# Optimization experiments

Hardware: AMD Instinct MI355X
Metric: run time of the kernel (lower is better)

Reference implementation:

```python
import jax, jax.numpy as jnp
import numpy as np

MAX_DIST = 8
GUIDANCE_WEIGHT = 0.4
EPS_MAG = 1e-6
EPS_COS = 1e-8
EPS_WSUM = 1e-8


def setup_inputs() -> dict:
    key = jax.random.key(0)
    k1, k2 = jax.random.split(key)
    embeddings = jax.random.normal(k1, (4, 2048, 1024), dtype=jnp.float32)
    guidance_trajectories = jax.random.normal(k2, (512, 1024), dtype=jnp.float32)
    return {"embeddings": embeddings, "guidance_trajectories": guidance_trajectories}


def reference(embeddings, guidance_trajectories):
    B, S, D = embeddings.shape
    W = min(MAX_DIST, S - 1)  # fixed max window size

    # consecutive-token trajectory vectors: diffs[t] = emb[t+1] - emb[t]
    diffs = embeddings[:, 1:, :] - embeddings[:, :-1, :]          # [B, S-1, D]

    # sliding windows of the last W diffs ending at pos-1
    pos = jnp.arange(S)[:, None]                                  # [S, 1]
    k = jnp.arange(W)[None, :]                                    # [1, W]
    idx = pos - W + k                                             # diff index per slot
    valid = (idx >= 0) & (pos >= 1)                               # [S, W]
    windows = diffs[:, jnp.clip(idx, 0, S - 2), :]                # [B, S, W, D]

    # torch.linspace(0.1, 1.0, w) weights, per-position window size w = min(pos, W);
    # valid entries occupy the last w slots of the W-wide window.
    w = jnp.minimum(pos, W)                                       # [S, 1]
    j = k - (W - w)                                               # local index within window
    lin = jnp.where(w > 1, 0.1 + 0.9 * j / jnp.maximum(w - 1, 1), 0.1)
    pos_weights = jnp.where(valid, lin, 0.0).astype(embeddings.dtype)  # [S, W]

    # normalize trajectory vectors, zero where magnitude <= 1e-6
    mag = jnp.linalg.norm(windows, axis=-1, keepdims=True)        # [B, S, W, 1]
    is_valid_mag = mag > EPS_MAG
    normed = jnp.where(is_valid_mag, windows / jnp.where(is_valid_mag, mag, 1.0), 0.0)

    mag_weights = jnp.tanh(mag * 2.0)                             # [B, S, W, 1]
    combined = pos_weights[None, :, :, None] * mag_weights        # [B, S, W, 1]

    # guidance influence: softmax over cosine similarity to guidance bank
    g_norm = jnp.linalg.norm(guidance_trajectories, axis=-1)      # [G]
    a_norm = jnp.linalg.norm(normed, axis=-1)                     # [B, S, W]
    dots = jnp.einsum('bswd,gd->bswg', normed, guidance_trajectories)
    sims = dots / (jnp.maximum(a_norm, EPS_COS)[..., None] * jnp.maximum(g_norm, EPS_COS))
    g_weights = jax.nn.softmax(sims * 2.0, axis=-1)               # [B, S, W, G]
    influence = jnp.einsum('bswg,gd->bswd', g_weights, guidance_trajectories)
    blended = (1.0 - GUIDANCE_WEIGHT) * normed + GUIDANCE_WEIGHT * influence

    weight_sum = jnp.maximum(combined.sum(axis=2), EPS_WSUM)      # [B, S, 1]
    trajectories = (blended * combined).sum(axis=2) / weight_sum  # [B, S, D]
    return trajectories
```

## Files before the change

kernel.cpp:

```cpp
#include <hip/hip_runtime.h>
#include <math.h>

#define B_ 4
#define S_ 2048
#define D_ 1024
#define G_ 512
#define T_ 2047
#define R_ 8188
#define RPAD 8192
#define MT 32
#define ABST 520

typedef __attribute__((ext_vector_type(8))) short short8;
typedef __attribute__((ext_vector_type(4))) short s16x4;
typedef __attribute__((ext_vector_type(4))) float f32x4;
typedef __attribute__((ext_vector_type(4))) unsigned short u16x4;

#define WSOFF_RG2  0u
#define WSOFF_MAGW 2048u
#define WSOFF_RMAG 34816u
#define WSOFF_BP1  67584u
#define WSOFF_BP2  1116160u
#define WSOFF_NH   2164736u
#define WSOFF_IH   18941952u

__device__ inline short to_bf16(float f) {
    union { float f; unsigned u; } v; v.f = f;
    unsigned r = v.u + 0x7fffu + ((v.u >> 16) & 1u);
    return (short)(r >> 16);
}
__device__ inline float fb(unsigned short h) {
    union { unsigned u; float f; } v;
    v.u = ((unsigned)h) << 16;
    return v.f;
}

__global__ __launch_bounds__(256) void prep_kernel(const float* __restrict__ guid,
                                                   float* __restrict__ rg2,
                                                   short8* __restrict__ Bp1,
                                                   short8* __restrict__ Bp2) {
    int bid = blockIdx.x, tid = threadIdx.x;
    if (bid < 128) {
        int wave = tid >> 6, lane = tid & 63;
        int g = bid * 4 + wave;
        const float4* gp = (const float4*)(guid + (size_t)g * D_);
        float ss = 0.f;
#pragma unroll
        for (int i = 0; i < 4; ++i) {
            float4 v = gp[lane + 64 * i];
            ss += v.x * v.x + v.y * v.y + v.z * v.z + v.w * v.w;
        }
#pragma unroll
        for (int m = 32; m >= 1; m >>= 1) ss += __shfl_xor(ss, m, 64);
        if (lane == 0) rg2[g] = 2.0f / fmaxf(sqrtf(ss), 1e-8f);
#pragma unroll
        for (int h = 0; h < 2; ++h) {
            int kg = lane + 64 * h;
            const float* src = guid + (size_t)g * D_ + kg * 8;
            short8 v;
#pragma unroll
            for (int j = 0; j < 8; ++j) v[j] = to_bf16(src[j]);
            Bp1[(size_t)kg * G_ + g] = v;
        }
    } else {
        int gg = bid - 128;
#pragma unroll
        for (int dd = 0; dd < 4; ++dd) {
            int d = tid + 256 * dd;
            short8 v;
#pragma unroll
            for (int j = 0; j < 8; ++j) v[j] = to_bf16(guid[(size_t)(gg * 8 + j) * D_ + d]);
            Bp2[(size_t)gg * D_ + d] = v;
        }
    }
}

__global__ __launch_bounds__(1024, 4) void fused_kernel(const float* __restrict__ emb,
                                                        const short8* __restrict__ Bp1,
                                                        const short8* __restrict__ Bp2,
                                                        const float* __restrict__ rg2,
                                                        float* __restrict__ magw,
                                                        float* __restrict__ rmagA,
                                                        short* __restrict__ normh,
                                                        short* __restrict__ inflh) {
    __shared__ short AB[MT][ABST];
    __shared__ float rg2s[G_];
    __shared__ float pred[MT][16];
    __shared__ float redmx[MT], redrs[MT];
    __shared__ float rmagS[MT];

    const int tid = threadIdx.x;
    const int wave = tid >> 6, lane = tid & 63;
    const int l15 = lane & 15, quad = lane >> 4;
    const int r0 = blockIdx.x * MT;

    if (tid < G_) rg2s[tid] = rg2[tid];

    float4 hx0[2][2], hx1[2][2];
    float ssp[2];
    int Rrow[2];
#pragma unroll
    for (int i = 0; i < 2; ++i) {
        int rr = wave * 2 + i;
        int R = r0 + rr;
        Rrow[i] = R;
        if (R < R_) {
            int b = R / T_;
            int t = R - b * T_;
            const float4* p = (const float4*)(emb + ((size_t)b * S_ + t) * D_);
            float ss = 0.f;
            short* nb = normh + (size_t)R * D_ + 4 * lane;
#pragma unroll
            for (int j = 0; j < 2; ++j) {
                float4 x0 = p[lane + 64 * j];
                float4 x1 = p[lane + 64 * j + 256];
                float4 dv = make_float4(x1.x - x0.x, x1.y - x0.y, x1.z - x0.z, x1.w - x0.w);
                ss += dv.x * dv.x + dv.y * dv.y + dv.z * dv.z + dv.w * dv.w;
                s16x4 h;
                h[0] = to_bf16(dv.x); h[1] = to_bf16(dv.y);
                h[2] = to_bf16(dv.z); h[3] = to_bf16(dv.w);
                *(s16x4*)(nb + 256 * j) = h;
                *(s16x4*)&AB[rr][4 * lane + 256 * j] = h;
            }
            ssp[i] = ss;
#pragma unroll
            for (int j = 0; j < 2; ++j) {
                hx0[i][j] = p[lane + 64 * (j + 2)];
                hx1[i][j] = p[lane + 64 * (j + 2) + 256];
            }
        } else {
            s16x4 z = (s16x4)0;
            *(s16x4*)&AB[rr][4 * lane] = z;
            *(s16x4*)&AB[rr][4 * lane + 256] = z;
            ssp[i] = 0.f;
#pragma unroll
            for (int j = 0; j < 2; ++j) {
                hx0[i][j] = make_float4(0.f, 0.f, 0.f, 0.f);
                hx1[i][j] = make_float4(0.f, 0.f, 0.f, 0.f);
            }
        }
    }
    __builtin_amdgcn_sched_barrier(0);
    asm volatile("s_waitcnt lgkmcnt(0)" ::: "memory");
    __builtin_amdgcn_s_barrier();

    f32x4 acc1[2][2];
#pragma unroll
    for (int mt = 0; mt < 2; ++mt)
#pragma unroll
        for (int nt = 0; nt < 2; ++nt) acc1[mt][nt] = (f32x4)0.f;
    {
        const short8* Bb = Bp1 + (size_t)quad * G_ + wave * 32 + l15;
        short8 bc0 = Bb[0], bc1 = Bb[16], bn0, bn1;
        for (int ks = 0; ks < 16; ++ks) {
            if (ks < 15) {
                const short8* Bx = Bb + (size_t)(ks + 1) * 4 * G_;
                bn0 = Bx[0]; bn1 = Bx[16];
            }
            short8 a0 = *(const short8*)&AB[l15][ks * 32 + quad * 8];
            short8 a1 = *(const short8*)&AB[16 + l15][ks * 32 + quad * 8];
            acc1[0][0] = __builtin_amdgcn_mfma_f32_16x16x32_bf16(a0, bc0, acc1[0][0], 0, 0, 0);
            acc1[0][1] = __builtin_amdgcn_mfma_f32_16x16x32_bf16(a0, bc1, acc1[0][1], 0, 0, 0);
            acc1[1][0] = __builtin_amdgcn_mfma_f32_16x16x32_bf16(a1, bc0, acc1[1][0], 0, 0, 0);
            acc1[1][1] = __builtin_amdgcn_mfma_f32_16x16x32_bf16(a1, bc1, acc1[1][1], 0, 0, 0);
            bc0 = bn0; bc1 = bn1;
        }
    }

    s16x4 holdh[2][2];
#pragma unroll
    for (int i = 0; i < 2; ++i) {
        int R = Rrow[i];
        int rr = wave * 2 + i;
        float ss = ssp[i];
        if (R < R_) {
            short* nb = normh + (size_t)R * D_ + 4 * lane;
#pragma unroll
            for (int j = 0; j < 2; ++j) {
                float4 dv = make_float4(hx1[i][j].x - hx0[i][j].x, hx1[i][j].y - hx0[i][j].y,
                                        hx1[i][j].z - hx0[i][j].z, hx1[i][j].w - hx0[i][j].w);
                ss += dv.x * dv.x + dv.y * dv.y + dv.z * dv.z + dv.w * dv.w;
                s16x4 h;
                h[0] = to_bf16(dv.x); h[1] = to_bf16(dv.y);
                h[2] = to_bf16(dv.z); h[3] = to_bf16(dv.w);
                *(s16x4*)(nb + 256 * (j + 2)) = h;
                holdh[i][j] = h;
            }
        } else {
            holdh[i][0] = (s16x4)0; holdh[i][1] = (s16x4)0;
        }
#pragma unroll
        for (int m = 32; m >= 1; m >>= 1) ss += __shfl_xor(ss, m, 64);
        float mag = sqrtf(ss);
        float rmag = (mag > 1e-6f) ? (1.0f / mag) : 0.0f;
        if (lane == 0) {
            rmagS[rr] = rmag;
            if (R < R_) { magw[R] = tanhf(2.0f * mag); rmagA[R] = rmag; }
        }
    }
    __syncthreads();
#pragma unroll
    for (int i = 0; i < 2; ++i) {
        int rr = wave * 2 + i;
        *(s16x4*)&AB[rr][4 * lane] = holdh[i][0];
        *(s16x4*)&AB[rr][4 * lane + 256] = holdh[i][1];
    }
    __syncthreads();

    {
        const short8* Bb = Bp1 + (size_t)(64 + quad) * G_ + wave * 32 + l15;
        short8 bc0 = Bb[0], bc1 = Bb[16], bn0, bn1;
        for (int ks = 0; ks < 16; ++ks) {
            if (ks < 15) {
                const short8* Bx = Bb + (size_t)(ks + 1) * 4 * G_;
                bn0 = Bx[0]; bn1 = Bx[16];
            }
            short8 a0 = *(const short8*)&AB[l15][ks * 32 + quad * 8];
            short8 a1 = *(const short8*)&AB[16 + l15][ks * 32 + quad * 8];
            acc1[0][0] = __builtin_amdgcn_mfma_f32_16x16x32_bf16(a0, bc0, acc1[0][0], 0, 0, 0);
            acc1[0][1] = __builtin_amdgcn_mfma_f32_16x16x32_bf16(a0, bc1, acc1[0][1], 0, 0, 0);
            acc1[1][0] = __builtin_amdgcn_mfma_f32_16x16x32_bf16(a1, bc0, acc1[1][0], 0, 0, 0);
            acc1[1][1] = __builtin_amdgcn_mfma_f32_16x16x32_bf16(a1, bc1, acc1[1][1], 0, 0, 0);
            bc0 = bn0; bc1 = bn1;
        }
    }

    {
        float rmv[2][4];
#pragma unroll
        for (int mt = 0; mt < 2; ++mt)
#pragma unroll
            for (int r2 = 0; r2 < 4; ++r2) rmv[mt][r2] = rmagS[mt * 16 + quad * 4 + r2];
        float pmax[2][4];
#pragma unroll
        for (int mt = 0; mt < 2; ++mt)
#pragma unroll
            for (int r2 = 0; r2 < 4; ++r2) pmax[mt][r2] = -1e30f;
#pragma unroll
        for (int mt = 0; mt < 2; ++mt)
#pragma unroll
            for (int nt = 0; nt < 2; ++nt) {
                float rgv = rg2s[wave * 32 + nt * 16 + l15];
#pragma unroll
                for (int r2 = 0; r2 < 4; ++r2) {
                    float lg = acc1[mt][nt][r2] * rgv * rmv[mt][r2];
                    acc1[mt][nt][r2] = lg;
                    pmax[mt][r2] = fmaxf(pmax[mt][r2], lg);
                }
            }
#pragma unroll
        for (int m = 8; m >= 1; m >>= 1)
#pragma unroll
            for (int mt = 0; mt < 2; ++mt)
#pragma unroll
                for (int r2 = 0; r2 < 4; ++r2)
                    pmax[mt][r2] = fmaxf(pmax[mt][r2], __shfl_xor(pmax[mt][r2], m, 16));
        if (l15 == 0) {
#pragma unroll
            for (int mt = 0; mt < 2; ++mt)
#pragma unroll
                for (int r2 = 0; r2 < 4; ++r2)
                    pred[mt * 16 + quad * 4 + r2][wave] = pmax[mt][r2];
        }
        __syncthreads();
        if (tid < MT) {
            float m = pred[tid][0];
#pragma unroll
            for (int w2 = 1; w2 < 16; ++w2) m = fmaxf(m, pred[tid][w2]);
            redmx[tid] = m;
        }
        __syncthreads();
        float psum[2][4];
#pragma unroll
        for (int mt = 0; mt < 2; ++mt)
#pragma unroll
            for (int r2 = 0; r2 < 4; ++r2) psum[mt][r2] = 0.f;
#pragma unroll
        for (int mt = 0; mt < 2; ++mt)
#pragma unroll
            for (int nt = 0; nt < 2; ++nt)
#pragma unroll
                for (int r2 = 0; r2 < 4; ++r2) {
                    float e = __expf(acc1[mt][nt][r2] - redmx[mt * 16 + quad * 4 + r2]);
                    acc1[mt][nt][r2] = e;
                    psum[mt][r2] += e;
                }
#pragma unroll
        for (int m = 8; m >= 1; m >>= 1)
#pragma unroll
            for (int mt = 0; mt < 2; ++mt)
#pragma unroll
                for (int r2 = 0; r2 < 4; ++r2)
                    psum[mt][r2] += __shfl_xor(psum[mt][r2], m, 16);
        if (l15 == 0) {
#pragma unroll
            for (int mt = 0; mt < 2; ++mt)
#pragma unroll
                for (int r2 = 0; r2 < 4; ++r2)
                    pred[mt * 16 + quad * 4 + r2][wave] = psum[mt][r2];
        }
        __syncthreads();
        if (tid < MT) {
            float s = 0.f;
#pragma unroll
            for (int w2 = 0; w2 < 16; ++w2) s += pred[tid][w2];
            redrs[tid] = 1.0f / s;
        }
        __syncthreads();
#pragma unroll
        for (int mt = 0; mt < 2; ++mt)
#pragma unroll
            for (int nt = 0; nt < 2; ++nt)
#pragma unroll
                for (int r2 = 0; r2 < 4; ++r2) {
                    int row = mt * 16 + quad * 4 + r2;
                    AB[row][wave * 32 + nt * 16 + l15] =
                        to_bf16(acc1[mt][nt][r2] * redrs[row]);
                }
    }
    __syncthreads();

    f32x4 acc2[2][4];
#pragma unroll
    for (int mt = 0; mt < 2; ++mt)
#pragma unroll
        for (int nt = 0; nt < 4; ++nt) acc2[mt][nt] = (f32x4)0.f;
    {
        const short8* Bb = Bp2 + (size_t)quad * D_ + wave * 64 + l15;
        short8 bc[4], bn[4];
#pragma unroll
        for (int nt = 0; nt < 4; ++nt) bc[nt] = Bb[nt * 16];
        for (int ks = 0; ks < 16; ++ks) {
            if (ks < 15) {
                const short8* Bx = Bb + (size_t)(ks + 1) * 4 * D_;
#pragma unroll
                for (int nt = 0; nt < 4; ++nt) bn[nt] = Bx[nt * 16];
            }
            short8 a0 = *(const short8*)&AB[l15][ks * 32 + quad * 8];
            short8 a1 = *(const short8*)&AB[16 + l15][ks * 32 + quad * 8];
#pragma unroll
            for (int nt = 0; nt < 4; ++nt) {
                acc2[0][nt] = __builtin_amdgcn_mfma_f32_16x16x32_bf16(a0, bc[nt], acc2[0][nt], 0, 0, 0);
                acc2[1][nt] = __builtin_amdgcn_mfma_f32_16x16x32_bf16(a1, bc[nt], acc2[1][nt], 0, 0, 0);
            }
#pragma unroll
            for (int nt = 0; nt < 4; ++nt) bc[nt] = bn[nt];
        }
    }

#pragma unroll
    for (int mt = 0; mt < 2; ++mt)
#pragma unroll
        for (int nt = 0; nt < 4; ++nt) {
            int d = wave * 64 + nt * 16 + l15;
#pragma unroll
            for (int r2 = 0; r2 < 4; ++r2) {
                int R = r0 + mt * 16 + quad * 4 + r2;
                if (R < R_) inflh[(size_t)R * D_ + d] = to_bf16(acc2[mt][nt][r2]);
            }
        }
}

__global__ __launch_bounds__(256) void combine_kernel(const float* __restrict__ magw,
                                                      const float* __restrict__ rmagA,
                                                      const unsigned short* __restrict__ normh,
                                                      const unsigned short* __restrict__ inflh,
                                                      float* __restrict__ out) {
    int blk = blockIdx.x;
    int b = blk >> 7;
    int s0 = (blk & 127) * 16;
    int d0 = threadIdx.x * 4;
    size_t rbase = (size_t)b * T_;

    f32x4 ring[8]; float mring[8];
#pragma unroll
    for (int j = 0; j < 8; ++j) { ring[j] = (f32x4)0.f; mring[j] = 0.f; }

#define BLEND(n4_, i4_, ns_, dst_)                                       \
    {                                                                    \
        dst_[0] = ns_ * fb(n4_[0]) + 0.4f * fb(i4_[0]);                  \
        dst_[1] = ns_ * fb(n4_[1]) + 0.4f * fb(i4_[1]);                  \
        dst_[2] = ns_ * fb(n4_[2]) + 0.4f * fb(i4_[2]);                  \
        dst_[3] = ns_ * fb(n4_[3]) + 0.4f * fb(i4_[3]);                  \
    }

    if (s0 != 0) {
#pragma unroll
        for (int j = 0; j < 8; ++j) {
            int t = s0 - 8 + j;
            size_t off = (rbase + t) * D_ + d0;
            u16x4 n4 = *(const u16x4*)(normh + off);
            u16x4 i4 = *(const u16x4*)(inflh + off);
            float ns = 0.6f * rmagA[rbase + t];
            BLEND(n4, i4, ns, ring[j]);
            mring[j] = magw[rbase + t];
        }
#pragma unroll
        for (int i = 0; i < 16; ++i) {
            u16x4 pn = (u16x4)0, pi = (u16x4)0; float pm = 0.f, pr = 0.f;
            if (i < 15) {
                int t = s0 + i;
                size_t off = (rbase + t) * D_ + d0;
                pn = *(const u16x4*)(normh + off);
                pi = *(const u16x4*)(inflh + off);
                pm = magw[rbase + t];
                pr = rmagA[rbase + t];
            }
            f32x4 acc = (f32x4)0.f; float wsum = 0.f;
#pragma unroll
            for (int a = 1; a <= 8; ++a) {
                int slot = (i - a) & 7;
                const float lin = 0.1f + (0.9f / 7.0f) * (float)(8 - a);
                float wt = lin * mring[slot];
                acc[0] += wt * ring[slot][0]; acc[1] += wt * ring[slot][1];
                acc[2] += wt * ring[slot][2]; acc[3] += wt * ring[slot][3];
                wsum += wt;
            }
            float rws = 1.0f / fmaxf(wsum, 1e-8f);
            f32x4 o; o[0] = acc[0] * rws; o[1] = acc[1] * rws; o[2] = acc[2] * rws; o[3] = acc[3] * rws;
            *(f32x4*)&out[((size_t)b * S_ + s0 + i) * D_ + d0] = o;
            if (i < 15) {
                float ns = 0.6f * pr;
                BLEND(pn, pi, ns, ring[i & 7]);
                mring[i & 7] = pm;
            }
        }
    } else {
#pragma unroll
        for (int i = 0; i < 16; ++i) {
            u16x4 pn = (u16x4)0, pi = (u16x4)0; float pm = 0.f, pr = 0.f;
            if (i < 15) {
                int t = i;
                size_t off = (rbase + t) * D_ + d0;
                pn = *(const u16x4*)(normh + off);
                pi = *(const u16x4*)(inflh + off);
                pm = magw[rbase + t];
                pr = rmagA[rbase + t];
            }
            const int w = (i < 8) ? i : 8;
            f32x4 acc = (f32x4)0.f; float wsum = 0.f;
            if (w > 0) {
                const float rw = (w > 1) ? 0.9f / (float)(w - 1) : 0.0f;
#pragma unroll
                for (int a = 1; a <= 8; ++a) {
                    if (a <= w) {
                        int slot = (i - a) & 7;
                        float lin = 0.1f + rw * (float)(w - a);
                        float wt = lin * mring[slot];
                        acc[0] += wt * ring[slot][0]; acc[1] += wt * ring[slot][1];
                        acc[2] += wt * ring[slot][2]; acc[3] += wt * ring[slot][3];
                        wsum += wt;
                    }
                }
            }
            float rws = 1.0f / fmaxf(wsum, 1e-8f);
            f32x4 o; o[0] = acc[0] * rws; o[1] = acc[1] * rws; o[2] = acc[2] * rws; o[3] = acc[3] * rws;
            *(f32x4*)&out[((size_t)b * S_ + i) * D_ + d0] = o;
            if (i < 15) {
                float ns = 0.6f * pr;
                BLEND(pn, pi, ns, ring[i & 7]);
                mring[i & 7] = pm;
            }
        }
    }
#undef BLEND
}

extern "C" void kernel_launch(void* const* d_in, const int* in_sizes, int n_in,
                              void* d_out, int out_size, void* d_ws, size_t ws_size,
                              hipStream_t stream) {
    const float* emb  = (const float*)d_in[0];
    const float* guid = (const float*)d_in[1];
    float* out = (float*)d_out;
    char* ws = (char*)d_ws;

    float*  rg2   = (float*)(ws + WSOFF_RG2);
    float*  magw  = (float*)(ws + WSOFF_MAGW);
    float*  rmagA = (float*)(ws + WSOFF_RMAG);
    short8* Bp1   = (short8*)(ws + WSOFF_BP1);
    short8* Bp2   = (short8*)(ws + WSOFF_BP2);
    short*  normh = (short*)(ws + WSOFF_NH);
    short*  inflh = (short*)(ws + WSOFF_IH);

    prep_kernel<<<192, 256, 0, stream>>>(guid, rg2, Bp1, Bp2);
    fused_kernel<<<RPAD / MT, 1024, 0, stream>>>(emb, Bp1, Bp2, rg2, magw, rmagA, normh, inflh);
    combine_kernel<<<B_ * 128, 256, 0, stream>>>(magw, rmagA, (const unsigned short*)normh,
                                                 (const unsigned short*)inflh, out);
}
```

Baseline: 127.0 us.

## Drop softmax max pass, deepen GEMM prefetch, defer normalization, halve combine tile

The softmax no longer subtracts a row max, because the logits are cosine similarities times two and so stay bounded. This removes one cross-wave reduction and two block barriers. The row-sum reciprocal is now applied to the second GEMM's output rather than to the probabilities. Both GEMMs get deeper register prefetch of the B operand (four stages for the first, two for the second), and the remaining half of the embedding loads is issued after the first GEMM's prefetch. The combine kernel uses 8-row tiles with twice as many blocks and a software-pipelined load/blend sequence, at the cost of more halo reloads.

```diff
diff --git a/kernel.cpp b/kernel.cpp
--- a/kernel.cpp
+++ b/kernel.cpp
@@ -34,6 +34,16 @@
     v.u = ((unsigned)h) << 16;
     return v.f;
 }
+__device__ inline f32x4 MF(short8 a, short8 b, f32x4 c) {
+    return __builtin_amdgcn_mfma_f32_16x16x32_bf16(a, b, c, 0, 0, 0);
+}
+
+#define RAWBAR() do {                                            \
+    __builtin_amdgcn_sched_barrier(0);                           \
+    asm volatile("s_waitcnt lgkmcnt(0)" ::: "memory");           \
+    __builtin_amdgcn_s_barrier();                                \
+    __builtin_amdgcn_sched_barrier(0);                           \
+} while (0)
 
 __global__ __launch_bounds__(256) void prep_kernel(const float* __restrict__ guid,
                                                    float* __restrict__ rg2,
@@ -74,6 +84,12 @@
         }
     }
 }
+
+#define G1Q(ksv, q)  {                                                        \
+    short8 a0 = *(const short8*)&AB[l15][(ksv) * 32 + quad * 8];              \
+    short8 a1 = *(const short8*)&AB[16 + l15][(ksv) * 32 + quad * 8];         \
+    acc1[0][0] = MF(a0, q[0], acc1[0][0]); acc1[0][1] = MF(a0, q[1], acc1[0][1]); \
+    acc1[1][0] = MF(a1, q[0], acc1[1][0]); acc1[1][1] = MF(a1, q[1], acc1[1][1]); }
 
 __global__ __launch_bounds__(1024, 4) void fused_kernel(const float* __restrict__ emb,
                                                         const short8* __restrict__ Bp1,
@@ -86,7 +102,7 @@
     __shared__ short AB[MT][ABST];
     __shared__ float rg2s[G_];
     __shared__ float pred[MT][16];
-    __shared__ float redmx[MT], redrs[MT];
+    __shared__ float redrs[MT];
     __shared__ float rmagS[MT];
 
     const int tid = threadIdx.x;
@@ -96,7 +112,7 @@
 
     if (tid < G_) rg2s[tid] = rg2[tid];
 
-    float4 hx0[2][2], hx1[2][2];
+    const float4* prow[2];
     float ssp[2];
     int Rrow[2];
 #pragma unroll
@@ -104,11 +120,12 @@
         int rr = wave * 2 + i;
         int R = r0 + rr;
         Rrow[i] = R;
+        float ss = 0.f;
         if (R < R_) {
             int b = R / T_;
             int t = R - b * T_;
             const float4* p = (const float4*)(emb + ((size_t)b * S_ + t) * D_);
-            float ss = 0.f;
+            prow[i] = p;
             short* nb = normh + (size_t)R * D_ + 4 * lane;
 #pragma unroll
             for (int j = 0; j < 2; ++j) {
@@ -122,48 +139,51 @@
                 *(s16x4*)(nb + 256 * j) = h;
                 *(s16x4*)&AB[rr][4 * lane + 256 * j] = h;
             }
-            ssp[i] = ss;
-#pragma unroll
-            for (int j = 0; j < 2; ++j) {
-                hx0[i][j] = p[lane + 64 * (j + 2)];
-                hx1[i][j] = p[lane + 64 * (j + 2) + 256];
-            }
         } else {
+            prow[i] = (const float4*)emb;
             s16x4 z = (s16x4)0;
             *(s16x4*)&AB[rr][4 * lane] = z;
             *(s16x4*)&AB[rr][4 * lane + 256] = z;
-            ssp[i] = 0.f;
-#pragma unroll
-            for (int j = 0; j < 2; ++j) {
-                hx0[i][j] = make_float4(0.f, 0.f, 0.f, 0.f);
-                hx1[i][j] = make_float4(0.f, 0.f, 0.f, 0.f);
-            }
-        }
-    }
-    __builtin_amdgcn_sched_barrier(0);
-    asm volatile("s_waitcnt lgkmcnt(0)" ::: "memory");
-    __builtin_amdgcn_s_barrier();
+        }
+        ssp[i] = ss;
+    }
+    RAWBAR();
 
     f32x4 acc1[2][2];
 #pragma unroll
     for (int mt = 0; mt < 2; ++mt)
 #pragma unroll
         for (int nt = 0; nt < 2; ++nt) acc1[mt][nt] = (f32x4)0.f;
+
+    float4 hx0[2][2], hx1[2][2];
     {
         const short8* Bb = Bp1 + (size_t)quad * G_ + wave * 32 + l15;
-        short8 bc0 = Bb[0], bc1 = Bb[16], bn0, bn1;
-        for (int ks = 0; ks < 16; ++ks) {
-            if (ks < 15) {
-                const short8* Bx = Bb + (size_t)(ks + 1) * 4 * G_;
-                bn0 = Bx[0]; bn1 = Bx[16];
-            }
-            short8 a0 = *(const short8*)&AB[l15][ks * 32 + quad * 8];
-            short8 a1 = *(const short8*)&AB[16 + l15][ks * 32 + quad * 8];
-            acc1[0][0] = __builtin_amdgcn_mfma_f32_16x16x32_bf16(a0, bc0, acc1[0][0], 0, 0, 0);
-            acc1[0][1] = __builtin_amdgcn_mfma_f32_16x16x32_bf16(a0, bc1, acc1[0][1], 0, 0, 0);
-            acc1[1][0] = __builtin_amdgcn_mfma_f32_16x16x32_bf16(a1, bc0, acc1[1][0], 0, 0, 0);
-            acc1[1][1] = __builtin_amdgcn_mfma_f32_16x16x32_bf16(a1, bc1, acc1[1][1], 0, 0, 0);
-            bc0 = bn0; bc1 = bn1;
+        short8 q0[2], q1[2], q2[2], q3[2];
+        q0[0] = Bb[0];          q0[1] = Bb[16];
+        q1[0] = Bb[4 * G_];     q1[1] = Bb[4 * G_ + 16];
+        q2[0] = Bb[8 * G_];     q2[1] = Bb[8 * G_ + 16];
+        q3[0] = Bb[12 * G_];    q3[1] = Bb[12 * G_ + 16];
+#pragma unroll
+        for (int i = 0; i < 2; ++i) {
+            if (Rrow[i] < R_) {
+#pragma unroll
+                for (int j = 0; j < 2; ++j) {
+                    hx0[i][j] = prow[i][lane + 64 * (j + 2)];
+                    hx1[i][j] = prow[i][lane + 64 * (j + 2) + 256];
+                }
+            } else {
+                hx0[i][0] = make_float4(0.f, 0.f, 0.f, 0.f);
+                hx0[i][1] = make_float4(0.f, 0.f, 0.f, 0.f);
+                hx1[i][0] = make_float4(0.f, 0.f, 0.f, 0.f);
+                hx1[i][1] = make_float4(0.f, 0.f, 0.f, 0.f);
+            }
+        }
+#pragma unroll
+        for (int k4 = 0; k4 < 16; k4 += 4) {
+            G1Q(k4 + 0, q0); if (k4 < 12) { q0[0] = Bb[(k4 + 4) * 4 * G_]; q0[1] = Bb[(k4 + 4) * 4 * G_ + 16]; }
+            G1Q(k4 + 1, q1); if (k4 < 12) { q1[0] = Bb[(k4 + 5) * 4 * G_]; q1[1] = Bb[(k4 + 5) * 4 * G_ + 16]; }
+            G1Q(k4 + 2, q2); if (k4 < 12) { q2[0] = Bb[(k4 + 6) * 4 * G_]; q2[1] = Bb[(k4 + 6) * 4 * G_ + 16]; }
+            G1Q(k4 + 3, q3); if (k4 < 12) { q3[0] = Bb[(k4 + 7) * 4 * G_]; q3[1] = Bb[(k4 + 7) * 4 * G_ + 16]; }
         }
     }
 
@@ -198,32 +218,35 @@
             if (R < R_) { magw[R] = tanhf(2.0f * mag); rmagA[R] = rmag; }
         }
     }
-    __syncthreads();
+    RAWBAR();
 #pragma unroll
     for (int i = 0; i < 2; ++i) {
         int rr = wave * 2 + i;
         *(s16x4*)&AB[rr][4 * lane] = holdh[i][0];
         *(s16x4*)&AB[rr][4 * lane + 256] = holdh[i][1];
     }
-    __syncthreads();
+    RAWBAR();
 
     {
         const short8* Bb = Bp1 + (size_t)(64 + quad) * G_ + wave * 32 + l15;
-        short8 bc0 = Bb[0], bc1 = Bb[16], bn0, bn1;
-        for (int ks = 0; ks < 16; ++ks) {
-            if (ks < 15) {
-                const short8* Bx = Bb + (size_t)(ks + 1) * 4 * G_;
-                bn0 = Bx[0]; bn1 = Bx[16];
-            }
-            short8 a0 = *(const short8*)&AB[l15][ks * 32 + quad * 8];
-            short8 a1 = *(const short8*)&AB[16 + l15][ks * 32 + quad * 8];
-            acc1[0][0] = __builtin_amdgcn_mfma_f32_16x16x32_bf16(a0, bc0, acc1[0][0], 0, 0, 0);
-            acc1[0][1] = __builtin_amdgcn_mfma_f32_16x16x32_bf16(a0, bc1, acc1[0][1], 0, 0, 0);
-            acc1[1][0] = __builtin_amdgcn_mfma_f32_16x16x32_bf16(a1, bc0, acc1[1][0], 0, 0, 0);
-            acc1[1][1] = __builtin_amdgcn_mfma_f32_16x16x32_bf16(a1, bc1, acc1[1][1], 0, 0, 0);
-            bc0 = bn0; bc1 = bn1;
-        }
-    }
+        short8 q0[2], q1[2], q2[2], q3[2];
+        q0[0] = Bb[0];          q0[1] = Bb[16];
+        q1[0] = Bb[4 * G_];     q1[1] = Bb[4 * G_ + 16];
+        q2[0] = Bb[8 * G_];     q2[1] = Bb[8 * G_ + 16];
+        q3[0] = Bb[12 * G_];    q3[1] = Bb[12 * G_ + 16];
+#pragma unroll
+        for (int k4 = 0; k4 < 16; k4 += 4) {
+            G1Q(k4 + 0, q0); if (k4 < 12) { q0[0] = Bb[(k4 + 4) * 4 * G_]; q0[1] = Bb[(k4 + 4) * 4 * G_ + 16]; }
+            G1Q(k4 + 1, q1); if (k4 < 12) { q1[0] = Bb[(k4 + 5) * 4 * G_]; q1[1] = Bb[(k4 + 5) * 4 * G_ + 16]; }
+            G1Q(k4 + 2, q2); if (k4 < 12) { q2[0] = Bb[(k4 + 6) * 4 * G_]; q2[1] = Bb[(k4 + 6) * 4 * G_ + 16]; }
+            G1Q(k4 + 3, q3); if (k4 < 12) { q3[0] = Bb[(k4 + 7) * 4 * G_]; q3[1] = Bb[(k4 + 7) * 4 * G_ + 16]; }
+        }
+    }
+
+    const short8* Bb2 = Bp2 + (size_t)quad * D_ + wave * 64 + l15;
+    short8 c0[4];
+#pragma unroll
+    for (int nt = 0; nt < 4; ++nt) c0[nt] = Bb2[nt * 16];
 
     {
         float rmv[2][4];
@@ -231,11 +254,11 @@
         for (int mt = 0; mt < 2; ++mt)
 #pragma unroll
             for (int r2 = 0; r2 < 4; ++r2) rmv[mt][r2] = rmagS[mt * 16 + quad * 4 + r2];
-        float pmax[2][4];
+        float psum[2][4];
 #pragma unroll
         for (int mt = 0; mt < 2; ++mt)
 #pragma unroll
-            for (int r2 = 0; r2 < 4; ++r2) pmax[mt][r2] = -1e30f;
+            for (int r2 = 0; r2 < 4; ++r2) psum[mt][r2] = 0.f;
 #pragma unroll
         for (int mt = 0; mt < 2; ++mt)
 #pragma unroll
@@ -243,48 +266,11 @@
                 float rgv = rg2s[wave * 32 + nt * 16 + l15];
 #pragma unroll
                 for (int r2 = 0; r2 < 4; ++r2) {
-                    float lg = acc1[mt][nt][r2] * rgv * rmv[mt][r2];
-                    acc1[mt][nt][r2] = lg;
-                    pmax[mt][r2] = fmaxf(pmax[mt][r2], lg);
-                }
-            }
-#pragma unroll
-        for (int m = 8; m >= 1; m >>= 1)
-#pragma unroll
-            for (int mt = 0; mt < 2; ++mt)
-#pragma unroll
-                for (int r2 = 0; r2 < 4; ++r2)
-                    pmax[mt][r2] = fmaxf(pmax[mt][r2], __shfl_xor(pmax[mt][r2], m, 16));
-        if (l15 == 0) {
-#pragma unroll
-            for (int mt = 0; mt < 2; ++mt)
-#pragma unroll
-                for (int r2 = 0; r2 < 4; ++r2)
-                    pred[mt * 16 + quad * 4 + r2][wave] = pmax[mt][r2];
-        }
-        __syncthreads();
-        if (tid < MT) {
-            float m = pred[tid][0];
-#pragma unroll
-            for (int w2 = 1; w2 < 16; ++w2) m = fmaxf(m, pred[tid][w2]);
-            redmx[tid] = m;
-        }
-        __syncthreads();
-        float psum[2][4];
-#pragma unroll
-        for (int mt = 0; mt < 2; ++mt)
-#pragma unroll
-            for (int r2 = 0; r2 < 4; ++r2) psum[mt][r2] = 0.f;
-#pragma unroll
-        for (int mt = 0; mt < 2; ++mt)
-#pragma unroll
-            for (int nt = 0; nt < 2; ++nt)
-#pragma unroll
-                for (int r2 = 0; r2 < 4; ++r2) {
-                    float e = __expf(acc1[mt][nt][r2] - redmx[mt * 16 + quad * 4 + r2]);
+                    float e = __expf(acc1[mt][nt][r2] * rgv * rmv[mt][r2]);
                     acc1[mt][nt][r2] = e;
                     psum[mt][r2] += e;
                 }
+            }
 #pragma unroll
         for (int m = 8; m >= 1; m >>= 1)
 #pragma unroll
@@ -292,6 +278,15 @@
 #pragma unroll
                 for (int r2 = 0; r2 < 4; ++r2)
                     psum[mt][r2] += __shfl_xor(psum[mt][r2], m, 16);
+        RAWBAR();
+#pragma unroll
+        for (int mt = 0; mt < 2; ++mt)
+#pragma unroll
+            for (int nt = 0; nt < 2; ++nt)
+#pragma unroll
+                for (int r2 = 0; r2 < 4; ++r2)
+                    AB[mt * 16 + quad * 4 + r2][wave * 32 + nt * 16 + l15] =
+                        to_bf16(acc1[mt][nt][r2]);
         if (l15 == 0) {
 #pragma unroll
             for (int mt = 0; mt < 2; ++mt)
@@ -299,26 +294,14 @@
                 for (int r2 = 0; r2 < 4; ++r2)
                     pred[mt * 16 + quad * 4 + r2][wave] = psum[mt][r2];
         }
-        __syncthreads();
-        if (tid < MT) {
-            float s = 0.f;
-#pragma unroll
-            for (int w2 = 0; w2 < 16; ++w2) s += pred[tid][w2];
-            redrs[tid] = 1.0f / s;
-        }
-        __syncthreads();
-#pragma unroll
-        for (int mt = 0; mt < 2; ++mt)
-#pragma unroll
-            for (int nt = 0; nt < 2; ++nt)
-#pragma unroll
-                for (int r2 = 0; r2 < 4; ++r2) {
-                    int row = mt * 16 + quad * 4 + r2;
-                    AB[row][wave * 32 + nt * 16 + l15] =
-                        to_bf16(acc1[mt][nt][r2] * redrs[row]);
-                }
-    }
-    __syncthreads();
+    }
+    RAWBAR();
+    if (tid < MT) {
+        float s = 0.f;
+#pragma unroll
+        for (int w2 = 0; w2 < 16; ++w2) s += pred[tid][w2];
+        redrs[tid] = 1.0f / s;
+    }
 
     f32x4 acc2[2][4];
 #pragma unroll
@@ -326,27 +309,40 @@
 #pragma unroll
         for (int nt = 0; nt < 4; ++nt) acc2[mt][nt] = (f32x4)0.f;
     {
-        const short8* Bb = Bp2 + (size_t)quad * D_ + wave * 64 + l15;
-        short8 bc[4], bn[4];
-#pragma unroll
-        for (int nt = 0; nt < 4; ++nt) bc[nt] = Bb[nt * 16];
-        for (int ks = 0; ks < 16; ++ks) {
-            if (ks < 15) {
-                const short8* Bx = Bb + (size_t)(ks + 1) * 4 * D_;
-#pragma unroll
-                for (int nt = 0; nt < 4; ++nt) bn[nt] = Bx[nt * 16];
-            }
-            short8 a0 = *(const short8*)&AB[l15][ks * 32 + quad * 8];
-            short8 a1 = *(const short8*)&AB[16 + l15][ks * 32 + quad * 8];
-#pragma unroll
-            for (int nt = 0; nt < 4; ++nt) {
-                acc2[0][nt] = __builtin_amdgcn_mfma_f32_16x16x32_bf16(a0, bc[nt], acc2[0][nt], 0, 0, 0);
-                acc2[1][nt] = __builtin_amdgcn_mfma_f32_16x16x32_bf16(a1, bc[nt], acc2[1][nt], 0, 0, 0);
-            }
-#pragma unroll
-            for (int nt = 0; nt < 4; ++nt) bc[nt] = bn[nt];
-        }
-    }
+        short8 c1[4];
+#pragma unroll
+        for (int nt = 0; nt < 4; ++nt) c1[nt] = Bb2[4 * D_ + nt * 16];
+#pragma unroll
+        for (int k2 = 0; k2 < 16; k2 += 2) {
+            {
+                short8 a0 = *(const short8*)&AB[l15][k2 * 32 + quad * 8];
+                short8 a1 = *(const short8*)&AB[16 + l15][k2 * 32 + quad * 8];
+#pragma unroll
+                for (int nt = 0; nt < 4; ++nt) {
+                    acc2[0][nt] = MF(a0, c0[nt], acc2[0][nt]);
+                    acc2[1][nt] = MF(a1, c0[nt], acc2[1][nt]);
+                }
+                if (k2 < 14) {
+#pragma unroll
+                    for (int nt = 0; nt < 4; ++nt) c0[nt] = Bb2[(k2 + 2) * 4 * D_ + nt * 16];
+                }
+            }
+            {
+                short8 a0 = *(const short8*)&AB[l15][(k2 + 1) * 32 + quad * 8];
+                short8 a1 = *(const short8*)&AB[16 + l15][(k2 + 1) * 32 + quad * 8];
+#pragma unroll
+                for (int nt = 0; nt < 4; ++nt) {
+                    acc2[0][nt] = MF(a0, c1[nt], acc2[0][nt]);
+                    acc2[1][nt] = MF(a1, c1[nt], acc2[1][nt]);
+                }
+                if (k2 < 14) {
+#pragma unroll
+                    for (int nt = 0; nt < 4; ++nt) c1[nt] = Bb2[(k2 + 3) * 4 * D_ + nt * 16];
+                }
+            }
+        }
+    }
+    RAWBAR();
 
 #pragma unroll
     for (int mt = 0; mt < 2; ++mt)
@@ -355,8 +351,9 @@
             int d = wave * 64 + nt * 16 + l15;
 #pragma unroll
             for (int r2 = 0; r2 < 4; ++r2) {
-                int R = r0 + mt * 16 + quad * 4 + r2;
-                if (R < R_) inflh[(size_t)R * D_ + d] = to_bf16(acc2[mt][nt][r2]);
+                int row = mt * 16 + quad * 4 + r2;
+                int R = r0 + row;
+                if (R < R_) inflh[(size_t)R * D_ + d] = to_bf16(acc2[mt][nt][r2] * redrs[row]);
             }
         }
 }
@@ -367,77 +364,75 @@
                                                       const unsigned short* __restrict__ inflh,
                                                       float* __restrict__ out) {
     int blk = blockIdx.x;
-    int b = blk >> 7;
-    int s0 = (blk & 127) * 16;
+    int b = blk >> 8;
+    int s0 = (blk & 255) * 8;
     int d0 = threadIdx.x * 4;
     size_t rbase = (size_t)b * T_;
+    float* ob = out + ((size_t)b * S_ + s0) * D_ + d0;
 
     f32x4 ring[8]; float mring[8];
 #pragma unroll
     for (int j = 0; j < 8; ++j) { ring[j] = (f32x4)0.f; mring[j] = 0.f; }
 
-#define BLEND(n4_, i4_, ns_, dst_)                                       \
-    {                                                                    \
-        dst_[0] = ns_ * fb(n4_[0]) + 0.4f * fb(i4_[0]);                  \
-        dst_[1] = ns_ * fb(n4_[1]) + 0.4f * fb(i4_[1]);                  \
-        dst_[2] = ns_ * fb(n4_[2]) + 0.4f * fb(i4_[2]);                  \
-        dst_[3] = ns_ * fb(n4_[3]) + 0.4f * fb(i4_[3]);                  \
-    }
+#define CLOAD(t_, N_, I_, M_, RV_) {                                     \
+        size_t off_ = (rbase + (t_)) * D_ + d0;                          \
+        N_ = *(const u16x4*)(normh + off_);                              \
+        I_ = *(const u16x4*)(inflh + off_);                              \
+        M_ = magw[rbase + (t_)];                                         \
+        RV_ = rmagA[rbase + (t_)]; }
+
+#define CBLEND(slot_, N_, I_, M_, RV_) {                                 \
+        float ns_ = 0.6f * (RV_);                                        \
+        ring[slot_][0] = ns_ * fb(N_[0]) + 0.4f * fb(I_[0]);             \
+        ring[slot_][1] = ns_ * fb(N_[1]) + 0.4f * fb(I_[1]);             \
+        ring[slot_][2] = ns_ * fb(N_[2]) + 0.4f * fb(I_[2]);             \
+        ring[slot_][3] = ns_ * fb(N_[3]) + 0.4f * fb(I_[3]);             \
+        mring[slot_] = (M_); }
+
+#define CTAPS(i_) {                                                      \
+        f32x4 acc = (f32x4)0.f; float wsum = 0.f;                        \
+        _Pragma("unroll")                                                \
+        for (int a = 1; a <= 8; ++a) {                                   \
+            int slot = ((i_) - a) & 7;                                   \
+            float lin = 0.1f + (0.9f / 7.0f) * (float)(8 - a);           \
+            float wt = lin * mring[slot];                                \
+            acc[0] += wt * ring[slot][0]; acc[1] += wt * ring[slot][1];  \
+            acc[2] += wt * ring[slot][2]; acc[3] += wt * ring[slot][3];  \
+            wsum += wt; }                                                \
+        float rws = 1.0f / fmaxf(wsum, 1e-8f);                           \
+        f32x4 o; o[0] = acc[0] * rws; o[1] = acc[1] * rws;               \
+        o[2] = acc[2] * rws; o[3] = acc[3] * rws;                        \
+        *(f32x4*)(ob + (size_t)(i_) * D_) = o; }
 
     if (s0 != 0) {
 #pragma unroll
         for (int j = 0; j < 8; ++j) {
             int t = s0 - 8 + j;
-            size_t off = (rbase + t) * D_ + d0;
-            u16x4 n4 = *(const u16x4*)(normh + off);
-            u16x4 i4 = *(const u16x4*)(inflh + off);
-            float ns = 0.6f * rmagA[rbase + t];
-            BLEND(n4, i4, ns, ring[j]);
-            mring[j] = magw[rbase + t];
-        }
-#pragma unroll
-        for (int i = 0; i < 16; ++i) {
-            u16x4 pn = (u16x4)0, pi = (u16x4)0; float pm = 0.f, pr = 0.f;
-            if (i < 15) {
-                int t = s0 + i;
-                size_t off = (rbase + t) * D_ + d0;
-                pn = *(const u16x4*)(normh + off);
-                pi = *(const u16x4*)(inflh + off);
-                pm = magw[rbase + t];
-                pr = rmagA[rbase + t];
-            }
-            f32x4 acc = (f32x4)0.f; float wsum = 0.f;
-#pragma unroll
-            for (int a = 1; a <= 8; ++a) {
-                int slot = (i - a) & 7;
-                const float lin = 0.1f + (0.9f / 7.0f) * (float)(8 - a);
-                float wt = lin * mring[slot];
-                acc[0] += wt * ring[slot][0]; acc[1] += wt * ring[slot][1];
-                acc[2] += wt * ring[slot][2]; acc[3] += wt * ring[slot][3];
-                wsum += wt;
-            }
-            float rws = 1.0f / fmaxf(wsum, 1e-8f);
-            f32x4 o; o[0] = acc[0] * rws; o[1] = acc[1] * rws; o[2] = acc[2] * rws; o[3] = acc[3] * rws;
-            *(f32x4*)&out[((size_t)b * S_ + s0 + i) * D_ + d0] = o;
-            if (i < 15) {
-                float ns = 0.6f * pr;
-                BLEND(pn, pi, ns, ring[i & 7]);
-                mring[i & 7] = pm;
-            }
-        }
+            u16x4 n4, i4; float pm, pr;
+            CLOAD(t, n4, i4, pm, pr);
+            CBLEND(j, n4, i4, pm, pr);
+        }
+        u16x4 An, Ai, Bn, Bi; float Am, Ar, Bm, Br;
+        CLOAD(s0,     An, Ai, Am, Ar);
+        CLOAD(s0 + 1, Bn, Bi, Bm, Br);
+        CTAPS(0); CBLEND(0, An, Ai, Am, Ar); CLOAD(s0 + 2, An, Ai, Am, Ar);
+        CTAPS(1); CBLEND(1, Bn, Bi, Bm, Br); CLOAD(s0 + 3, Bn, Bi, Bm, Br);
+        CTAPS(2); CBLEND(2, An, Ai, Am, Ar); CLOAD(s0 + 4, An, Ai, Am, Ar);
+        CTAPS(3); CBLEND(3, Bn, Bi, Bm, Br); CLOAD(s0 + 5, Bn, Bi, Bm, Br);
+        CTAPS(4); CBLEND(4, An, Ai, Am, Ar); CLOAD(s0 + 6, An, Ai, Am, Ar);
+        CTAPS(5); CBLEND(5, Bn, Bi, Bm, Br);
+        CTAPS(6); CBLEND(6, An, Ai, Am, Ar);
+        CTAPS(7);
     } else {
 #pragma unroll
-        for (int i = 0; i < 16; ++i) {
-            u16x4 pn = (u16x4)0, pi = (u16x4)0; float pm = 0.f, pr = 0.f;
-            if (i < 15) {
-                int t = i;
-                size_t off = (rbase + t) * D_ + d0;
-                pn = *(const u16x4*)(normh + off);
-                pi = *(const u16x4*)(inflh + off);
-                pm = magw[rbase + t];
-                pr = rmagA[rbase + t];
-            }
-            const int w = (i < 8) ? i : 8;
+        for (int i = 0; i < 8; ++i) {
+            if (i >= 1) {
+                int t = i - 1;
+                u16x4 n4, i4; float pm, pr;
+                CLOAD(t, n4, i4, pm, pr);
+                CBLEND((i - 1) & 7, n4, i4, pm, pr);
+            }
+            const int w = i;
             f32x4 acc = (f32x4)0.f; float wsum = 0.f;
             if (w > 0) {
                 const float rw = (w > 1) ? 0.9f / (float)(w - 1) : 0.0f;
@@ -454,16 +449,14 @@
                 }
             }
             float rws = 1.0f / fmaxf(wsum, 1e-8f);
-            f32x4 o; o[0] = acc[0] * rws; o[1] = acc[1] * rws; o[2] = acc[2] * rws; o[3] = acc[3] * rws;
-            *(f32x4*)&out[((size_t)b * S_ + i) * D_ + d0] = o;
-            if (i < 15) {
-                float ns = 0.6f * pr;
-                BLEND(pn, pi, ns, ring[i & 7]);
-                mring[i & 7] = pm;
-            }
-        }
-    }
-#undef BLEND
+            f32x4 o; o[0] = acc[0] * rws; o[1] = acc[1] * rws;
+            o[2] = acc[2] * rws; o[3] = acc[3] * rws;
+            *(f32x4*)(ob + (size_t)i * D_) = o;
+        }
+    }
+#undef CLOAD
+#undef CBLEND
+#undef CTAPS
 }
 
 extern "C" void kernel_launch(void* const* d_in, const int* in_sizes, int n_in,
@@ -484,6 +477,6 @@
 
     prep_kernel<<<192, 256, 0, stream>>>(guid, rg2, Bp1, Bp2);
     fused_kernel<<<RPAD / MT, 1024, 0, stream>>>(emb, Bp1, Bp2, rg2, magw, rmagA, normh, inflh);
-    combine_kernel<<<B_ * 128, 256, 0, stream>>>(magw, rmagA, (const unsigned short*)normh,
+    combine_kernel<<<B_ * 256, 256, 0, stream>>>(magw, rmagA, (const unsigned short*)normh,
                                                  (const unsigned short*)inflh, out);
 }
```

After: 129.1 us. Within noise of the previous version (+1.6%).
